# Performance work log

Measured on AMD Instinct MI355X. Metric: run time of the kernel, lower is better.

The kernel has to match this reference:

```python
import jax, jax.numpy as jnp
import numpy as np

VOCAB = 50000
EMB = 300
HID = 300
LAYERS = 2
NTAGS = 11  # tags 0..8 are real labels, 9=START, 10=STOP
START = NTAGS - 2
STOP = NTAGS - 1
NEG = -10000.0


def _lstm_params(key, in_dim, hid):
    k = 1.0 / np.sqrt(hid)
    ks = jax.random.split(key, 4)
    u = lambda kk, shp: jax.random.uniform(kk, shp, jnp.float32, -k, k)
    return {
        'Wi': u(ks[0], (4 * hid, in_dim)),
        'Wh': u(ks[1], (4 * hid, hid)),
        'bi': u(ks[2], (4 * hid,)),
        'bh': u(ks[3], (4 * hid,)),
    }


def _run_lstm(p, xs, reverse=False):
    # xs: [T, B, D] -> [T, B, H]
    B = xs.shape[1]
    H = p['Wh'].shape[1]
    pre = jnp.einsum('tbd,gd->tbg', xs, p['Wi']) + p['bi'] + p['bh']

    def step(carry, pre_t):
        h, c = carry
        g = pre_t + h @ p['Wh'].T
        i, f, gg, o = jnp.split(g, 4, axis=-1)
        i = jax.nn.sigmoid(i)
        f = jax.nn.sigmoid(f)
        gg = jnp.tanh(gg)
        o = jax.nn.sigmoid(o)
        c = f * c + i * gg
        h = o * jnp.tanh(c)
        return (h, c), h

    init = (jnp.zeros((B, H), xs.dtype), jnp.zeros((B, H), xs.dtype))
    _, hs = jax.lax.scan(step, init, pre, reverse=reverse)
    return hs


def setup_inputs() -> dict:
    key = jax.random.key(0)
    ks = jax.random.split(key, 12)
    x = jax.random.randint(ks[0], (64, 512), 0, VOCAB, dtype=jnp.int32)
    emb = jax.random.normal(ks[1], (VOCAB, EMB), jnp.float32) * 0.02
    lstm = []
    ki = 2
    for layer in range(LAYERS):
        in_dim = EMB if layer == 0 else 2 * HID
        fwd = _lstm_params(ks[ki], in_dim, HID); ki += 1
        bwd = _lstm_params(ks[ki], in_dim, HID); ki += 1
        lstm.append((fwd, bwd))
    Wout = jax.random.normal(ks[ki], (NTAGS, 2 * HID), jnp.float32) * 0.02
    bout = jnp.zeros((NTAGS,), jnp.float32)
    trans = jax.random.normal(ks[ki + 1], (NTAGS, NTAGS), jnp.float32) * 0.1
    # transitions[i, j] = score of transitioning TO i FROM j
    trans = trans.at[START, :].set(NEG).at[:, STOP].set(NEG)
    params = {'emb': emb, 'Wout': Wout, 'bout': bout, 'trans': trans}
    for li, (f, b) in enumerate(lstm):
        for nm, d in (('f', f), ('b', b)):
            for k2, v in d.items():
                params[f'l{li}{nm}_{k2}'] = v
    return {'x': x, **params}


def _features(x, params):
    h = params['emb'][x]  # [B,T,E]
    h = jnp.transpose(h, (1, 0, 2))  # [T,B,E]
    for li in range(LAYERS):
        pf = {k2: params[f'l{li}f_{k2}'] for k2 in ('Wi', 'Wh', 'bi', 'bh')}
        pb = {k2: params[f'l{li}b_{k2}'] for k2 in ('Wi', 'Wh', 'bi', 'bh')}
        hf = _run_lstm(pf, h)
        hb = _run_lstm(pb, h, reverse=True)
        h = jnp.concatenate([hf, hb], axis=-1)  # [T,B,2H]
    feats = jnp.einsum('tbh,gh->tbg', h, params['Wout']) + params['bout']
    return feats  # [T,B,NTAGS]


def _viterbi(feats, trans):
    # feats: [T,B,K]; trans[i,j]: to i from j
    T, B, K = feats.shape
    init = jnp.full((B, K), NEG, feats.dtype).at[:, START].set(0.0)

    def step(fv, feat_t):
        # scores[b, i, j] = fv[b, j] + trans[i, j]
        scores = fv[:, None, :] + trans[None, :, :]
        bp = jnp.argmax(scores, axis=-1)  # [B,K]
        fv_new = jnp.max(scores, axis=-1) + feat_t
        return fv_new, bp

    fv, bps = jax.lax.scan(step, init, feats)  # bps: [T,B,K]
    term = fv + trans[STOP][None, :]
    best_last = jnp.argmax(term, axis=-1)  # [B]
    path_score = jnp.max(term, axis=-1)

    def back(tag, bp_t):
        prev = jnp.take_along_axis(bp_t, tag[:, None], axis=-1)[:, 0]
        return prev, tag

    _, path = jax.lax.scan(back, best_last, bps, reverse=True)  # [T,B]
    return path_score, jnp.transpose(path)  # [B], [B,T]


def reference(x, emb, Wout, bout, trans,
              l0f_Wi, l0f_Wh, l0f_bi, l0f_bh, l0b_Wi, l0b_Wh, l0b_bi, l0b_bh,
              l1f_Wi, l1f_Wh, l1f_bi, l1f_bh, l1b_Wi, l1b_Wh, l1b_bi, l1b_bh):
    params = dict(emb=emb, Wout=Wout, bout=bout, trans=trans,
                  l0f_Wi=l0f_Wi, l0f_Wh=l0f_Wh, l0f_bi=l0f_bi, l0f_bh=l0f_bh,
                  l0b_Wi=l0b_Wi, l0b_Wh=l0b_Wh, l0b_bi=l0b_bi, l0b_bh=l0b_bh,
                  l1f_Wi=l1f_Wi, l1f_Wh=l1f_Wh, l1f_bi=l1f_bi, l1f_bh=l1f_bh,
                  l1b_Wi=l1b_Wi, l1b_Wh=l1b_Wh, l1b_bi=l1b_bi, l1b_bh=l1b_bh)
    feats = _features(x, params)
    path_score, path = _viterbi(feats, trans)
    return path_score, path
```

## Files before the change

kernel.cpp:

```cpp
#include <hip/hip_runtime.h>
#include <hip/hip_bf16.h>

#define T_SEQ 512
#define NBATCH 64
#define HID 300
#define G4 1200
#define NTAG 11
#define TAG_START 9
#define TAG_STOP 10
#define NEGV -10000.0f
#define NWGD 38
#define NKT 10
#define HXE (40*2*64*8)
#define FLGS 16
#define FLGN 152
#define FLGDIR (FLGN*FLGS)
#define SSTEP 16
#define NCOMP 80

typedef unsigned short u16;
using short8 = __attribute__((ext_vector_type(8))) short;
using f32x4  = __attribute__((ext_vector_type(4))) float;
using f32x16 = __attribute__((ext_vector_type(16))) float;
using i32x4  = __attribute__((ext_vector_type(4))) int;

#define MF(a, b, c)   __builtin_amdgcn_mfma_f32_16x16x32_bf16((a), (b), (c), 0, 0, 0)
#define MF32(a, b, c) __builtin_amdgcn_mfma_f32_32x32x16_bf16((a), (b), (c), 0, 0, 0)

__device__ __forceinline__ float sigf(float x) { return 1.0f / (1.0f + expf(-x)); }

__device__ __forceinline__ u16 f2bf(float x) {
    unsigned u = __float_as_uint(x);
    unsigned r = (u + 0x7FFFu + ((u >> 16) & 1u)) >> 16;
    return (u16)r;
}
__device__ __forceinline__ float bf2f(u16 h) {
    return __uint_as_float((unsigned)h << 16);
}
__device__ __forceinline__ f32x16 zero16() {
    f32x16 z = {0.f,0.f,0.f,0.f,0.f,0.f,0.f,0.f,0.f,0.f,0.f,0.f,0.f,0.f,0.f,0.f};
    return z;
}

__device__ __forceinline__ i32x4 ld_cc_x4(const u16* p) {
    i32x4 r;
    asm volatile("global_load_dwordx4 %0, %1, off sc0 sc1" : "=v"(r) : "v"(p) : "memory");
    return r;
}
__device__ __forceinline__ unsigned ld_cc_b32(const unsigned* p) {
    unsigned r;
    asm volatile("global_load_dword %0, %1, off sc0 sc1\n\t"
                 "s_waitcnt vmcnt(0)" : "=v"(r) : "v"(p) : "memory");
    return r;
}
__device__ __forceinline__ void st_cc_x4(u16* p, i32x4 v) {
    asm volatile("global_store_dwordx4 %0, %1, off sc0 sc1" :: "v"(p), "v"(v) : "memory");
}
__device__ __forceinline__ void st_cc_b32(unsigned* p, unsigned v) {
    asm volatile("global_store_dword %0, %1, off sc0 sc1" :: "v"(p), "v"(v) : "memory");
}
__device__ __forceinline__ void wait_vm0() {
    asm volatile("s_waitcnt vmcnt(0)" ::: "memory");
}

__global__ __launch_bounds__(256) void k_gather(const int* __restrict__ x,
                                                const float* __restrict__ emb,
                                                u16* __restrict__ xs0)
{
    int t = blockIdx.x;
    __shared__ int rid[NBATCH];
    if (threadIdx.x < NBATCH) rid[threadIdx.x] = x[threadIdx.x * T_SEQ + t];
    __syncthreads();
    for (int o = threadIdx.x; o < 64 * 40; o += 256) {
        int b = o / 40, m8 = o - b * 40;
        unsigned hw[4], lw[4];
#pragma unroll
        for (int p = 0; p < 4; ++p) {
            int k0 = m8 * 8 + p * 2;
            float v0 = (k0 < 300)     ? emb[(size_t)rid[b] * 300 + k0]     : 0.0f;
            float v1 = (k0 + 1 < 300) ? emb[(size_t)rid[b] * 300 + k0 + 1] : 0.0f;
            u16 h0 = f2bf(v0), h1 = f2bf(v1);
            u16 l0 = f2bf(v0 - bf2f(h0)), l1 = f2bf(v1 - bf2f(h1));
            hw[p] = (unsigned)h0 | ((unsigned)h1 << 16);
            lw[p] = (unsigned)l0 | ((unsigned)l1 << 16);
        }
        u16* dst = xs0 + (((size_t)t * 40 + m8) * 64 + b) * 16;
        *(i32x4*)dst       = i32x4{(int)hw[0], (int)hw[1], (int)hw[2], (int)hw[3]};
        *(i32x4*)(dst + 8) = i32x4{(int)lw[0], (int)lw[1], (int)lw[2], (int)lw[3]};
    }
}

__global__ __launch_bounds__(256) void k_zpad(u16* __restrict__ xs1)
{
    int t = blockIdx.x;
    i32x4* base = (i32x4*)(xs1 + (((size_t)t * 80 + 76) * 64) * 16);
    i32x4 z = {0, 0, 0, 0};
    for (int o = threadIdx.x; o < 4 * 64 * 2; o += 256) base[o] = z;
}

template<int NKS, int KMAXW>
__device__ __forceinline__ void pregemm3_role(
    const u16* __restrict__ xs, int TNB,
    const float* __restrict__ Wi,
    float* __restrict__ pre,
    int jquad, int dir, int t0f, int t0b, int s0, int s1, int tid)
{
    int wv = tid >> 6, l = tid & 63;
    int jb = jquad * 4 + wv;
    int lo5 = l & 31, hi5 = l >> 5;

    short8 aH2[NKS], aL2[NKS];
    {
        int g = lo5 & 3, uo = lo5 >> 2;
        int jrow = jb * 8 + uo;
        bool jok = jrow < 300;
        const float* wr = Wi + ((size_t)g * 300 + (jok ? jrow : 0)) * KMAXW;
#pragma unroll
        for (int ks = 0; ks < NKS; ++ks) {
            short8 vh, vl;
#pragma unroll
            for (int e = 0; e < 8; ++e) {
                int u = ks * 16 + hi5 * 8 + e;
                bool valid; int cc;
                if (KMAXW == 600) { valid = jok && ((u < 300) || (u >= 304 && u < 604)); cc = (u < 300) ? u : u - 4; }
                else              { valid = jok && (u < 300); cc = u; }
                float w = valid ? wr[cc] : 0.0f;
                u16 hb = f2bf(w);
                vh[e] = (short)hb;
                vl[e] = (short)f2bf(w - bf2f(hb));
            }
            aH2[ks] = vh; aL2[ks] = vl;
        }
    }

    for (int s = s0; s < s1; ++s) {
        int t = dir ? (t0b - s) : (t0f + s);
        const u16* bt = xs + ((size_t)t * TNB * 64) * 16;
        float* po = pre + (size_t)s * (G4 * 64);
#pragma unroll
        for (int bh2 = 0; bh2 < 2; ++bh2) {
            int bcol = bh2 * 32 + lo5;
            f32x16 aA = zero16(), aB = zero16(), aC = zero16();
#pragma unroll
            for (int ks = 0; ks < NKS; ++ks) {
                const u16* gp = bt + ((size_t)(2 * ks + hi5) * 64 + bcol) * 16;
                short8 bhv = *(const short8*)gp;
                short8 blv = *(const short8*)(gp + 8);
                aA = MF32(aH2[ks], bhv, aA);
                aB = MF32(aL2[ks], bhv, aB);
                aC = MF32(aH2[ks], blv, aC);
            }
#pragma unroll
            for (int r = 0; r < 16; ++r) {
                int m = (r & 3) + 8 * (r >> 2) + 4 * hi5;
                int gg = m & 3, u2 = m >> 2;
                int jr = jb * 8 + u2;
                if (jr < 300)
                    po[(gg * 300 + jr) * 64 + bcol] = aA[r] + aB[r] + aC[r];
            }
        }
    }
}

template<int NKS, int KMAXW>
__global__ __launch_bounds__(256, 1) void k_pregemm3(
    const u16* __restrict__ xs, int TNB,
    const float* __restrict__ WiF, const float* __restrict__ WiB,
    float* __restrict__ preF, float* __restrict__ preB,
    int t0f, int t0b, int NSL, int C)
{
    int bx = blockIdx.x;
    int u = bx / NSL, sl = bx - u * NSL;
    int dir = u & 1, jquad = u >> 1;
    int s0 = sl * SSTEP, s1 = min(s0 + SSTEP, C);
    pregemm3_role<NKS, KMAXW>(xs, TNB, dir ? WiB : WiF,
        dir ? preB : preF, jquad, dir, t0f, t0b, s0, s1, threadIdx.x);
}

template<int MODE>
__device__ __forceinline__ void lstm_role(
    const float* __restrict__ preF, const float* __restrict__ preB,
    const float* __restrict__ WhF, const float* __restrict__ WhB,
    const float* __restrict__ biF, const float* __restrict__ bhF,
    const float* __restrict__ biB, const float* __restrict__ bhB,
    u16* __restrict__ hx, float* __restrict__ cbuf,
    float* __restrict__ xs2, u16* __restrict__ xs1,
    int t0f, int t0b, int C, int first,
    unsigned* __restrict__ flags,
    volatile unsigned* wgprog,
    int bid, int tid)
{
    __builtin_amdgcn_s_setprio(1);
    int dir = bid & 1, idx = bid >> 1;
    const float* pre = dir ? preB : preF;
    const float* Wh  = dir ? WhB : WhF;
    const float* biL = dir ? biB : biF;
    const float* bhL = dir ? bhB : bhF;
    u16* hxd = hx + (size_t)dir * 2 * HXE;
    float* cb = cbuf + (size_t)dir * 300 * 64;
    unsigned* flg = flags + (size_t)dir * FLGDIR;
    int w = tid >> 6, l = tid & 63;
    int hh = l >> 4, kbx = l >> 4;
    int bcol = w * 16 + (l & 15);
    int j0 = idx * 8;
    int ju0 = j0 + hh, ju1 = j0 + 4 + hh;
    int jc0 = min(ju0, 299), jc1 = min(ju1, 299);
    bool jv0 = ju0 < 300, jv1 = ju1 < 300;

    unsigned* myflag = flg + (size_t)(idx * 4 + w) * FLGS;
    const unsigned* shardp = flg + (size_t)(w * 38 + min(l, 37)) * FLGS;
    bool shact = l < 38;

    if (l == 0) wgprog[w] = 0;
    __syncthreads();

    short8 aH[2][NKT], aL[2][NKT];
    {
        int r = l & 15;
        int g = r & 3, uo = r >> 2;
#pragma unroll
        for (int q = 0; q < 2; ++q) {
            int jr = j0 + q * 4 + uo;
            const float* wr = Wh + ((size_t)g * 300 + min(jr, 299)) * 300;
            bool jvr = jr < 300;
#pragma unroll
            for (int kt = 0; kt < NKT; ++kt) {
                short8 vh, vl;
#pragma unroll
                for (int e = 0; e < 8; ++e) {
                    int k = kt * 32 + kbx * 8 + e;
                    float wv = (jvr && k < 300) ? wr[k] : 0.0f;
                    u16 hb = f2bf(wv);
                    vh[e] = (short)hb;
                    vl[e] = (short)f2bf(wv - bf2f(hb));
                }
                aH[q][kt] = vh; aL[q][kt] = vl;
            }
        }
    }
    float c0 = first ? 0.0f : cb[(size_t)jc0 * 64 + bcol];
    float c1 = first ? 0.0f : cb[(size_t)jc1 * 64 + bcol];

    float bias0[4], bias1[4];
#pragma unroll
    for (int g = 0; g < 4; ++g) {
        bias0[g] = biL[g * 300 + jc0] + bhL[g * 300 + jc0];
        bias1[g] = biL[g * 300 + jc1] + bhL[g * 300 + jc1];
    }

    float p0[4], p1[4];
#pragma unroll
    for (int g = 0; g < 4; ++g) {
        p0[g] = pre[((size_t)g * 300 + jc0) * 64 + bcol] + bias0[g];
        p1[g] = pre[((size_t)g * 300 + jc1) * 64 + bcol] + bias1[g];
    }

    int pp = 0;
    for (int s = 0; s < C; ++s) {
        f32x4 aA0 = {0.f,0.f,0.f,0.f}, aB0 = {0.f,0.f,0.f,0.f}, aC0 = {0.f,0.f,0.f,0.f};
        f32x4 aA1 = {0.f,0.f,0.f,0.f}, aB1 = {0.f,0.f,0.f,0.f}, aC1 = {0.f,0.f,0.f,0.f};
        if (!(first && s == 0)) {
            const u16* hxr = hxd + (size_t)pp * HXE;
            i32x4 bh[NKT], bl[NKT];
#pragma unroll
            for (int kt = 0; kt < NKT; ++kt) {
                const u16* gp = hxr + (size_t)(4 * kt + kbx) * 1024 + (size_t)bcol * 8;
                bh[kt] = ld_cc_x4(gp);
            }
#pragma unroll
            for (int kt = 0; kt < NKT; ++kt) {
                const u16* gp = hxr + (size_t)(4 * kt + kbx) * 1024 + (size_t)bcol * 8;
                bl[kt] = ld_cc_x4(gp + 512);
            }
            asm volatile("s_waitcnt vmcnt(10)" ::: "memory");
            __builtin_amdgcn_sched_barrier(0);
#pragma unroll
            for (int kt = 0; kt < NKT; ++kt) {
                short8 bhv = __builtin_bit_cast(short8, bh[kt]);
                aA0 = MF(aH[0][kt], bhv, aA0);
                aB0 = MF(aL[0][kt], bhv, aB0);
                aA1 = MF(aH[1][kt], bhv, aA1);
                aB1 = MF(aL[1][kt], bhv, aB1);
            }
            wait_vm0();
            __builtin_amdgcn_sched_barrier(0);
#pragma unroll
            for (int kt = 0; kt < NKT; ++kt) {
                short8 blv = __builtin_bit_cast(short8, bl[kt]);
                aC0 = MF(aH[0][kt], blv, aC0);
                aC1 = MF(aH[1][kt], blv, aC1);
            }
        }
        float hv0, hv1;
        {
            float gi = sigf(aA0[0] + aB0[0] + aC0[0] + p0[0]);
            float gf = sigf(aA0[1] + aB0[1] + aC0[1] + p0[1]);
            float gg = tanhf(aA0[2] + aB0[2] + aC0[2] + p0[2]);
            float go = sigf(aA0[3] + aB0[3] + aC0[3] + p0[3]);
            c0 = gf * c0 + gi * gg;
            hv0 = go * tanhf(c0);
            if (!jv0) hv0 = 0.0f;
        }
        {
            float gi = sigf(aA1[0] + aB1[0] + aC1[0] + p1[0]);
            float gf = sigf(aA1[1] + aB1[1] + aC1[1] + p1[1]);
            float gg = tanhf(aA1[2] + aB1[2] + aC1[2] + p1[2]);
            float go = sigf(aA1[3] + aB1[3] + aC1[3] + p1[3]);
            c1 = gf * c1 + gi * gg;
            hv1 = go * tanhf(c1);
            if (!jv1) hv1 = 0.0f;
        }
        u16 hb0 = f2bf(hv0);
        unsigned pk0 = (unsigned)hb0 | ((unsigned)f2bf(hv0 - bf2f(hb0)) << 16);
        u16 hb1 = f2bf(hv1);
        unsigned pk1 = (unsigned)hb1 | ((unsigned)f2bf(hv1 - bf2f(hb1)) << 16);
        int ls = l & 15;
        unsigned a0 = __shfl(pk0, ls), a1 = __shfl(pk0, ls + 16), a2 = __shfl(pk0, ls + 32), a3 = __shfl(pk0, ls + 48);
        unsigned b0 = __shfl(pk1, ls), b1 = __shfl(pk1, ls + 16), b2 = __shfl(pk1, ls + 32), b3 = __shfl(pk1, ls + 48);
        i32x4 hi4 = {(int)((a0 & 0xffffu) | (a1 << 16)), (int)((a2 & 0xffffu) | (a3 << 16)),
                     (int)((b0 & 0xffffu) | (b1 << 16)), (int)((b2 & 0xffffu) | (b3 << 16))};
        i32x4 lo4 = {(int)((a0 >> 16) | (a1 & 0xffff0000u)), (int)((a2 >> 16) | (a3 & 0xffff0000u)),
                     (int)((b0 >> 16) | (b1 & 0xffff0000u)), (int)((b2 >> 16) | (b3 & 0xffff0000u))};
        int t = dir ? (t0b - s) : (t0f + s);
        if (l < 16) {
            int b = w * 16 + l;
            u16* hxw = hxd + (size_t)(pp ^ 1) * HXE + (size_t)idx * 1024 + (size_t)b * 8;
            st_cc_x4(hxw, hi4);
            st_cc_x4(hxw + 512, lo4);
        }
        wait_vm0();
        if (l == 0) st_cc_b32(myflag, (unsigned)(s + 1));
        if (MODE == 0) {
            if (jv0) xs2[((size_t)t * 600 + dir * 300 + ju0) * 64 + bcol] = hv0;
            if (jv1) xs2[((size_t)t * 600 + dir * 300 + ju1) * 64 + bcol] = hv1;
        } else if (l < 16) {
            int b = w * 16 + l;
            u16* xd = xs1 + (((size_t)t * 80 + dir * 38 + idx) * 64 + b) * 16;
            *(i32x4*)xd       = hi4;
            *(i32x4*)(xd + 8) = lo4;
        }
        if (s + 1 < C) {
#pragma unroll
            for (int g = 0; g < 4; ++g) {
                p0[g] = pre[((size_t)(s + 1) * G4 + (size_t)g * 300 + jc0) * 64 + bcol] + bias0[g];
                p1[g] = pre[((size_t)(s + 1) * G4 + (size_t)g * 300 + jc1) * 64 + bcol] + bias1[g];
            }
            unsigned tgt = (unsigned)(s + 1);
            unsigned ok;
            do {
                unsigned v = tgt;
                if (shact) v = ld_cc_b32(shardp);
                ok = (v >= tgt) ? 1u : 0u;
            } while (!__all(ok));
            if (l == 0) wgprog[w] = tgt;
            while (!(wgprog[0] >= tgt && wgprog[1] >= tgt &&
                     wgprog[2] >= tgt && wgprog[3] >= tgt)) {
                __builtin_amdgcn_s_sleep(1);
            }
        }
        pp ^= 1;
    }
    if (jv0) cb[(size_t)jc0 * 64 + bcol] = c0;
    if (jv1) cb[(size_t)jc1 * 64 + bcol] = c1;
}

template<int NKS, int KMAXW, int MODE>
__global__ __launch_bounds__(256, 1) void k_chunk(
    const u16* __restrict__ xsN, int TNB,
    const float* __restrict__ WiF, const float* __restrict__ WiB,
    float* __restrict__ preNF, float* __restrict__ preNB,
    int t0fN, int t0bN, int do_pre, int CN, int NSLc,
    const float* __restrict__ preF, const float* __restrict__ preB,
    const float* __restrict__ WhF, const float* __restrict__ WhB,
    const float* __restrict__ biF, const float* __restrict__ bhF,
    const float* __restrict__ biB, const float* __restrict__ bhB,
    u16* __restrict__ hx, float* __restrict__ cbuf,
    float* __restrict__ xs2, u16* __restrict__ xs1,
    int t0f, int t0b, int C, int first,
    unsigned* __restrict__ flags)
{
    __shared__ unsigned wgprog[4];
    int bid = blockIdx.x;
    if (bid < 2 * NWGD) {
        lstm_role<MODE>(preF, preB, WhF, WhB, biF, bhF, biB, bhB, hx, cbuf,
                        xs2, xs1, t0f, t0b, C, first, flags, wgprog,
                        bid, threadIdx.x);
    } else if (do_pre) {
        int p = bid - 2 * NWGD;
        if (p < 20 * NSLc) {
            int u = p / NSLc, sl = p - u * NSLc;
            int dir = u & 1, jquad = u >> 1;
            int s0 = sl * SSTEP, s1 = min(s0 + SSTEP, CN);
            pregemm3_role<NKS, KMAXW>(xsN, TNB, dir ? WiB : WiF,
                dir ? preNB : preNF, jquad, dir, t0fN, t0bN, s0, s1, threadIdx.x);
        }
    }
}

__global__ __launch_bounds__(256) void k_feats(
    const float* __restrict__ xs2, const float* __restrict__ Wout,
    const float* __restrict__ bout, float* __restrict__ feats)
{
    int t = blockIdx.x;
    int tid = threadIdx.x;
    int b = tid & 63, g0 = tid >> 6;
    const float* xa = xs2 + (size_t)t * 600 * 64 + b;
    for (int g = g0; g < NTAG; g += 4) {
        float acc = bout[g];
        const float* wr = Wout + (size_t)g * 600;
#pragma unroll 4
        for (int k = 0; k < 600; ++k) acc += wr[k] * xa[(size_t)k * 64];
        feats[((size_t)t * NTAG + g) * 64 + b] = acc;
    }
}

__global__ __launch_bounds__(256) void k_viterbi(
    const float* __restrict__ feats, const float* __restrict__ trans,
    float* __restrict__ out)
{
    __shared__ unsigned char bp[4][T_SEQ * NTAG];
    int tid = threadIdx.x;
    int wv = tid >> 6, lane = tid & 63;
    int b = blockIdx.x * 4 + wv;
    int i = (lane < NTAG) ? lane : 0;
    bool act = lane < NTAG;
    float trow[NTAG];
#pragma unroll
    for (int j = 0; j < NTAG; ++j) trow[j] = trans[i * NTAG + j];
    float fv = (lane == TAG_START) ? 0.0f : NEGV;
    for (int t = 0; t < T_SEQ; ++t) {
        float m = -3.0e38f; int arg = 0;
#pragma unroll
        for (int j = 0; j < NTAG; ++j) {
            float fvj = __shfl(fv, j, 64);
            float sc = fvj + trow[j];
            if (sc > m) { m = sc; arg = j; }
        }
        float ft = feats[((size_t)t * NTAG + i) * 64 + b];
        fv = m + ft;
        if (act) bp[wv][t * NTAG + lane] = (unsigned char)arg;
    }
    float term = act ? (fv + trans[TAG_STOP * NTAG + i]) : -3.0e38f;
    int bi_ = lane;
#pragma unroll
    for (int off = 32; off >= 1; off >>= 1) {
        float ov = __shfl_xor(term, off, 64);
        int oi = __shfl_xor(bi_, off, 64);
        if (ov > term || (ov == term && oi < bi_)) { term = ov; bi_ = oi; }
    }
    if (lane == 0) {
        out[b] = term;
        int tag = bi_;
        float* po = out + 64 + (size_t)b * T_SEQ;
        for (int t = T_SEQ - 1; t >= 0; --t) {
            po[t] = (float)tag;
            tag = bp[wv][t * NTAG + tag];
        }
    }
}

extern "C" void kernel_launch(void* const* d_in, const int* in_sizes, int n_in,
                              void* d_out, int out_size, void* d_ws, size_t ws_size,
                              hipStream_t stream)
{
    (void)in_sizes; (void)n_in; (void)out_size;
    const int*   x     = (const int*)d_in[0];
    const float* emb   = (const float*)d_in[1];
    const float* Wout  = (const float*)d_in[2];
    const float* bout  = (const float*)d_in[3];
    const float* trans = (const float*)d_in[4];

    float* ws = (float*)d_ws;
    const size_t XS2F = (size_t)T_SEQ * 600 * NBATCH;
    const size_t XS1U = (size_t)T_SEQ * 80 * 64 * 16;
    const size_t FEA  = (size_t)T_SEQ * NTAG * NBATCH;

    float* xs2 = ws;
    u16* xs0 = (u16*)ws;
    u16* xs1 = (u16*)(ws + XS2F);
    float* featB = (float*)(xs1 + XS1U);
    float* cB = featB + FEA;
    u16* hxB = (u16*)(cB + 2 * 300 * 64);
    unsigned* flagsB = (unsigned*)(hxB + 4 * HXE);
    unsigned* padB = flagsB + 64ULL * 2 * FLGDIR;
    float* preBase = (float*)(padB + 16);
    size_t fixedBytes = (size_t)((char*)preBase - (char*)ws);

    int Cmax = 512;
    while (Cmax > 16 && fixedBytes + 16ULL * Cmax * G4 * NBATCH > ws_size) Cmax >>= 1;
    size_t Q = (size_t)Cmax * G4 * NBATCH;
    size_t slotF = 2 * Q;
    float* preS[2] = { preBase, preBase + slotF };

    int sizes[40], off[41], nch = 0;
    {
        int rem = T_SEQ;
        int f = (Cmax >= 64) ? 32 : Cmax;
        sizes[nch++] = f; rem -= f;
        while (rem > 0) { int s = rem < Cmax ? rem : Cmax; sizes[nch++] = s; rem -= s; }
        off[0] = 0;
        for (int i = 0; i < nch; ++i) off[i + 1] = off[i] + sizes[i];
    }

    (void)hipMemsetAsync(hxB, 0,
        4 * HXE * sizeof(u16) + (64ULL * 2 * FLGDIR) * sizeof(unsigned), stream);
    k_gather<<<T_SEQ, 256, 0, stream>>>(x, emb, xs0);
    k_zpad<<<T_SEQ, 256, 0, stream>>>(xs1);

    for (int layer = 0; layer < 2; ++layer) {
        int base = 5 + layer * 8;
        const float* WiF = (const float*)d_in[base + 0];
        const float* WhF = (const float*)d_in[base + 1];
        const float* biF = (const float*)d_in[base + 2];
        const float* bhF = (const float*)d_in[base + 3];
        const float* WiB = (const float*)d_in[base + 4];
        const float* WhB = (const float*)d_in[base + 5];
        const float* biB = (const float*)d_in[base + 6];
        const float* bhB = (const float*)d_in[base + 7];
        const u16* xsL = (layer == 0) ? xs0 : xs1;
        int TNB = (layer == 0) ? 40 : 80;

        {
            int NSL0 = (sizes[0] + SSTEP - 1) / SSTEP;
            if (layer == 0)
                k_pregemm3<20, 300><<<20 * NSL0, 256, 0, stream>>>(
                    xsL, TNB, WiF, WiB, preS[0], preS[0] + Q, 0, T_SEQ - 1, NSL0, sizes[0]);
            else
                k_pregemm3<40, 600><<<20 * NSL0, 256, 0, stream>>>(
                    xsL, TNB, WiF, WiB, preS[0], preS[0] + Q, 0, T_SEQ - 1, NSL0, sizes[0]);
        }

        for (int ci = 0; ci < nch; ++ci) {
            int cur = ci & 1, nxt = cur ^ 1;
            int t0f = off[ci], t0b = (T_SEQ - 1) - off[ci];
            int do_pre = (ci + 1 < nch) ? 1 : 0;
            int CN = do_pre ? sizes[ci + 1] : 0;
            int NSLc = do_pre ? (CN + SSTEP - 1) / SSTEP : 1;
            int t0fN = off[ci + 1], t0bN = (T_SEQ - 1) - off[ci + 1];
            int slot = layer * 32 + ci;
            unsigned* flags = flagsB + (size_t)slot * 2 * FLGDIR;
            float* pc = preS[cur];
            float* pn = preS[nxt];
            if (layer == 0)
                k_chunk<20, 300, 1><<<2 * NWGD + NCOMP, 256, 0, stream>>>(
                    xsL, TNB, WiF, WiB, pn, pn + Q, t0fN, t0bN, do_pre, CN, NSLc,
                    pc, pc + Q, WhF, WhB, biF, bhF, biB, bhB, hxB, cB,
                    xs2, xs1, t0f, t0b, sizes[ci], (ci == 0) ? 1 : 0, flags);
            else
                k_chunk<40, 600, 0><<<2 * NWGD + NCOMP, 256, 0, stream>>>(
                    xsL, TNB, WiF, WiB, pn, pn + Q, t0fN, t0bN, do_pre, CN, NSLc,
                    pc, pc + Q, WhF, WhB, biF, bhF, biB, bhB, hxB, cB,
                    xs2, xs1, t0f, t0b, sizes[ci], (ci == 0) ? 1 : 0, flags);
        }
    }
    k_feats<<<T_SEQ, 256, 0, stream>>>(xs2, Wout, bout, featB);
    k_viterbi<<<16, 256, 0, stream>>>(featB, trans, (float*)d_out);
}
```

Before: 7.063 ms.

## Split layer-1 input projection over K into two segments for more pregemm parallelism

```diff
diff --git a/kernel.cpp b/kernel.cpp
--- a/kernel.cpp
+++ b/kernel.cpp
@@ -98,13 +98,15 @@
     for (int o = threadIdx.x; o < 4 * 64 * 2; o += 256) base[o] = z;
 }
 
-template<int NKS, int KMAXW>
+template<int KMAXW>
 __device__ __forceinline__ void pregemm3_role(
     const u16* __restrict__ xs, int TNB,
     const float* __restrict__ Wi,
     float* __restrict__ pre,
-    int jquad, int dir, int t0f, int t0b, int s0, int s1, int tid)
-{
+    int jquad, int dir, int B0, int KOFF,
+    int t0f, int t0b, int s0, int s1, int tid)
+{
+    const int NKS = 20;
     int wv = tid >> 6, l = tid & 63;
     int jb = jquad * 4 + wv;
     int lo5 = l & 31, hi5 = l >> 5;
@@ -114,17 +116,14 @@
         int g = lo5 & 3, uo = lo5 >> 2;
         int jrow = jb * 8 + uo;
         bool jok = jrow < 300;
-        const float* wr = Wi + ((size_t)g * 300 + (jok ? jrow : 0)) * KMAXW;
+        const float* wr = Wi + ((size_t)g * 300 + (jok ? jrow : 0)) * KMAXW + KOFF;
 #pragma unroll
         for (int ks = 0; ks < NKS; ++ks) {
             short8 vh, vl;
 #pragma unroll
             for (int e = 0; e < 8; ++e) {
                 int u = ks * 16 + hi5 * 8 + e;
-                bool valid; int cc;
-                if (KMAXW == 600) { valid = jok && ((u < 300) || (u >= 304 && u < 604)); cc = (u < 300) ? u : u - 4; }
-                else              { valid = jok && (u < 300); cc = u; }
-                float w = valid ? wr[cc] : 0.0f;
+                float w = (jok && u < 300) ? wr[u] : 0.0f;
                 u16 hb = f2bf(w);
                 vh[e] = (short)hb;
                 vl[e] = (short)f2bf(w - bf2f(hb));
@@ -135,7 +134,7 @@
 
     for (int s = s0; s < s1; ++s) {
         int t = dir ? (t0b - s) : (t0f + s);
-        const u16* bt = xs + ((size_t)t * TNB * 64) * 16;
+        const u16* bt = xs + (((size_t)t * TNB + B0) * 64) * 16;
         float* po = pre + (size_t)s * (G4 * 64);
 #pragma unroll
         for (int bh2 = 0; bh2 < 2; ++bh2) {
@@ -162,24 +161,27 @@
     }
 }
 
-template<int NKS, int KMAXW>
+template<int KMAXW>
 __global__ __launch_bounds__(256, 1) void k_pregemm3(
     const u16* __restrict__ xs, int TNB,
     const float* __restrict__ WiF, const float* __restrict__ WiB,
-    float* __restrict__ preF, float* __restrict__ preB,
+    float* __restrict__ pbase, unsigned long long Q,
     int t0f, int t0b, int NSL, int C)
 {
     int bx = blockIdx.x;
     int u = bx / NSL, sl = bx - u * NSL;
-    int dir = u & 1, jquad = u >> 1;
+    int dir = u & 1, rest = u >> 1;
+    int seg = (rest >= 10) ? 1 : 0;
+    int jq = rest - seg * 10;
     int s0 = sl * SSTEP, s1 = min(s0 + SSTEP, C);
-    pregemm3_role<NKS, KMAXW>(xs, TNB, dir ? WiB : WiF,
-        dir ? preB : preF, jquad, dir, t0f, t0b, s0, s1, threadIdx.x);
+    pregemm3_role<KMAXW>(xs, TNB, dir ? WiB : WiF,
+        pbase + (size_t)(seg * 2 + dir) * Q, jq, dir, seg * 38, seg * 300,
+        t0f, t0b, s0, s1, threadIdx.x);
 }
 
 template<int MODE>
 __device__ __forceinline__ void lstm_role(
-    const float* __restrict__ preF, const float* __restrict__ preB,
+    const float* __restrict__ pc, unsigned long long Qc,
     const float* __restrict__ WhF, const float* __restrict__ WhB,
     const float* __restrict__ biF, const float* __restrict__ bhF,
     const float* __restrict__ biB, const float* __restrict__ bhB,
@@ -192,7 +194,8 @@
 {
     __builtin_amdgcn_s_setprio(1);
     int dir = bid & 1, idx = bid >> 1;
-    const float* pre = dir ? preB : preF;
+    const float* pre  = pc + (size_t)dir * Qc;
+    const float* pre2 = pc + (size_t)(2 + dir) * Qc;
     const float* Wh  = dir ? WhB : WhF;
     const float* biL = dir ? biB : biF;
     const float* bhL = dir ? bhB : bhF;
@@ -251,8 +254,11 @@
     float p0[4], p1[4];
 #pragma unroll
     for (int g = 0; g < 4; ++g) {
-        p0[g] = pre[((size_t)g * 300 + jc0) * 64 + bcol] + bias0[g];
-        p1[g] = pre[((size_t)g * 300 + jc1) * 64 + bcol] + bias1[g];
+        size_t o0 = ((size_t)g * 300 + jc0) * 64 + bcol;
+        size_t o1 = ((size_t)g * 300 + jc1) * 64 + bcol;
+        p0[g] = pre[o0] + bias0[g];
+        p1[g] = pre[o1] + bias1[g];
+        if (MODE == 0) { p0[g] += pre2[o0]; p1[g] += pre2[o1]; }
     }
 
     int pp = 0;
@@ -342,8 +348,11 @@
         if (s + 1 < C) {
 #pragma unroll
             for (int g = 0; g < 4; ++g) {
-                p0[g] = pre[((size_t)(s + 1) * G4 + (size_t)g * 300 + jc0) * 64 + bcol] + bias0[g];
-                p1[g] = pre[((size_t)(s + 1) * G4 + (size_t)g * 300 + jc1) * 64 + bcol] + bias1[g];
+                size_t o0 = ((size_t)(s + 1) * G4 + (size_t)g * 300 + jc0) * 64 + bcol;
+                size_t o1 = ((size_t)(s + 1) * G4 + (size_t)g * 300 + jc1) * 64 + bcol;
+                p0[g] = pre[o0] + bias0[g];
+                p1[g] = pre[o1] + bias1[g];
+                if (MODE == 0) { p0[g] += pre2[o0]; p1[g] += pre2[o1]; }
             }
             unsigned tgt = (unsigned)(s + 1);
             unsigned ok;
@@ -364,13 +373,13 @@
     if (jv1) cb[(size_t)jc1 * 64 + bcol] = c1;
 }
 
-template<int NKS, int KMAXW, int MODE>
+template<int KMAXW, int MODE>
 __global__ __launch_bounds__(256, 1) void k_chunk(
     const u16* __restrict__ xsN, int TNB,
     const float* __restrict__ WiF, const float* __restrict__ WiB,
-    float* __restrict__ preNF, float* __restrict__ preNB,
+    float* __restrict__ pn, unsigned long long Qn,
     int t0fN, int t0bN, int do_pre, int CN, int NSLc,
-    const float* __restrict__ preF, const float* __restrict__ preB,
+    const float* __restrict__ pc, unsigned long long Qc,
     const float* __restrict__ WhF, const float* __restrict__ WhB,
     const float* __restrict__ biF, const float* __restrict__ bhF,
     const float* __restrict__ biB, const float* __restrict__ bhB,
@@ -382,17 +391,21 @@
     __shared__ unsigned wgprog[4];
     int bid = blockIdx.x;
     if (bid < 2 * NWGD) {
-        lstm_role<MODE>(preF, preB, WhF, WhB, biF, bhF, biB, bhB, hx, cbuf,
+        lstm_role<MODE>(pc, Qc, WhF, WhB, biF, bhF, biB, bhB, hx, cbuf,
                         xs2, xs1, t0f, t0b, C, first, flags, wgprog,
                         bid, threadIdx.x);
     } else if (do_pre) {
+        const int NUNITS = (MODE == 0) ? 40 : 20;
         int p = bid - 2 * NWGD;
-        if (p < 20 * NSLc) {
+        if (p < NUNITS * NSLc) {
             int u = p / NSLc, sl = p - u * NSLc;
-            int dir = u & 1, jquad = u >> 1;
+            int dir = u & 1, rest = u >> 1;
+            int seg = (rest >= 10) ? 1 : 0;
+            int jq = rest - seg * 10;
             int s0 = sl * SSTEP, s1 = min(s0 + SSTEP, CN);
-            pregemm3_role<NKS, KMAXW>(xsN, TNB, dir ? WiB : WiF,
-                dir ? preNB : preNF, jquad, dir, t0fN, t0bN, s0, s1, threadIdx.x);
+            pregemm3_role<KMAXW>(xsN, TNB, dir ? WiB : WiF,
+                pn + (size_t)(seg * 2 + dir) * Qn, jq, dir, seg * 38, seg * 300,
+                t0fN, t0bN, s0, s1, threadIdx.x);
         }
     }
 }
@@ -488,19 +501,12 @@
 
     int Cmax = 512;
     while (Cmax > 16 && fixedBytes + 16ULL * Cmax * G4 * NBATCH > ws_size) Cmax >>= 1;
-    size_t Q = (size_t)Cmax * G4 * NBATCH;
-    size_t slotF = 2 * Q;
+    if (Cmax > 64) Cmax = 64;
+    int Cmax1 = Cmax >> 1;
+    size_t Q0 = (size_t)Cmax  * G4 * NBATCH;
+    size_t Q1 = (size_t)Cmax1 * G4 * NBATCH;
+    size_t slotF = 2 * Q0;
     float* preS[2] = { preBase, preBase + slotF };
-
-    int sizes[40], off[41], nch = 0;
-    {
-        int rem = T_SEQ;
-        int f = (Cmax >= 64) ? 32 : Cmax;
-        sizes[nch++] = f; rem -= f;
-        while (rem > 0) { int s = rem < Cmax ? rem : Cmax; sizes[nch++] = s; rem -= s; }
-        off[0] = 0;
-        for (int i = 0; i < nch; ++i) off[i + 1] = off[i] + sizes[i];
-    }
 
     (void)hipMemsetAsync(hxB, 0,
         4 * HXE * sizeof(u16) + (64ULL * 2 * FLGDIR) * sizeof(unsigned), stream);
@@ -519,15 +525,28 @@
         const float* bhB = (const float*)d_in[base + 7];
         const u16* xsL = (layer == 0) ? xs0 : xs1;
         int TNB = (layer == 0) ? 40 : 80;
+        int NSEG = (layer == 0) ? 1 : 2;
+        int CmaxL = (layer == 0) ? Cmax : Cmax1;
+        size_t QL = (layer == 0) ? Q0 : Q1;
+
+        int sizes[40], off[41], nch = 0;
+        {
+            int rem = T_SEQ;
+            int f = (CmaxL >= 64) ? 32 : CmaxL;
+            sizes[nch++] = f; rem -= f;
+            while (rem > 0) { int s = rem < CmaxL ? rem : CmaxL; sizes[nch++] = s; rem -= s; }
+            off[0] = 0;
+            for (int i = 0; i < nch; ++i) off[i + 1] = off[i] + sizes[i];
+        }
 
         {
             int NSL0 = (sizes[0] + SSTEP - 1) / SSTEP;
             if (layer == 0)
-                k_pregemm3<20, 300><<<20 * NSL0, 256, 0, stream>>>(
-                    xsL, TNB, WiF, WiB, preS[0], preS[0] + Q, 0, T_SEQ - 1, NSL0, sizes[0]);
+                k_pregemm3<300><<<NSEG * 20 * NSL0, 256, 0, stream>>>(
+                    xsL, TNB, WiF, WiB, preS[0], QL, 0, T_SEQ - 1, NSL0, sizes[0]);
             else
-                k_pregemm3<40, 600><<<20 * NSL0, 256, 0, stream>>>(
-                    xsL, TNB, WiF, WiB, preS[0], preS[0] + Q, 0, T_SEQ - 1, NSL0, sizes[0]);
+                k_pregemm3<600><<<NSEG * 20 * NSL0, 256, 0, stream>>>(
+                    xsL, TNB, WiF, WiB, preS[0], QL, 0, T_SEQ - 1, NSL0, sizes[0]);
         }
 
         for (int ci = 0; ci < nch; ++ci) {
@@ -542,14 +561,14 @@
             float* pc = preS[cur];
             float* pn = preS[nxt];
             if (layer == 0)
-                k_chunk<20, 300, 1><<<2 * NWGD + NCOMP, 256, 0, stream>>>(
-                    xsL, TNB, WiF, WiB, pn, pn + Q, t0fN, t0bN, do_pre, CN, NSLc,
-                    pc, pc + Q, WhF, WhB, biF, bhF, biB, bhB, hxB, cB,
+                k_chunk<300, 1><<<2 * NWGD + NCOMP, 256, 0, stream>>>(
+                    xsL, TNB, WiF, WiB, pn, QL, t0fN, t0bN, do_pre, CN, NSLc,
+                    pc, QL, WhF, WhB, biF, bhF, biB, bhB, hxB, cB,
                     xs2, xs1, t0f, t0b, sizes[ci], (ci == 0) ? 1 : 0, flags);
             else
-                k_chunk<40, 600, 0><<<2 * NWGD + NCOMP, 256, 0, stream>>>(
-                    xsL, TNB, WiF, WiB, pn, pn + Q, t0fN, t0bN, do_pre, CN, NSLc,
-                    pc, pc + Q, WhF, WhB, biF, bhF, biB, bhB, hxB, cB,
+                k_chunk<600, 0><<<2 * NWGD + NCOMP, 256, 0, stream>>>(
+                    xsL, TNB, WiF, WiB, pn, QL, t0fN, t0bN, do_pre, CN, NSLc,
+                    pc, QL, WhF, WhB, biF, bhF, biB, bhB, hxB, cB,
                     xs2, xs1, t0f, t0b, sizes[ci], (ci == 0) ? 1 : 0, flags);
         }
     }
```

New measurement: 6.410 ms. 1.1x faster.
